# Optimization experiments

Measured on AMD Instinct MI355X. Metric: run time of the kernel, lower is better.

The kernel has to match this reference:

```python
import jax, jax.numpy as jnp
import numpy as np

B, N, C, R = 4, 4096, 64, 16
EPS = 1e-12


def setup_inputs() -> dict:
    key = jax.random.key(0)
    k_x, k_w, k_u = jax.random.split(key, 3)
    x = jax.random.normal(k_x, (B, N, C), dtype=jnp.float32)
    W = jax.random.uniform(k_w, (B, N, N), dtype=jnp.float32)
    # lazily-initialized learnable low-rank factor U ~ 0.01 * randn(N, r)
    U = 0.01 * jax.random.normal(k_u, (N, R), dtype=jnp.float32)
    w_scale = jnp.asarray(1.0, dtype=jnp.float32)
    return {"x": x, "W": W, "U": U, "w_scale": w_scale}


def reference(x, W, U, w_scale):
    # symmetrize adjacency: W <- (W + W^T)/2
    Ws = 0.5 * (W + jnp.swapaxes(W, -1, -2))            # [B,N,N]
    # low-rank symmetric gate A = sigmoid(U U^T), shared over batch
    A = jax.nn.sigmoid(U @ U.T)                          # [N,N]
    K = Ws * A[None, :, :]                               # [B,N,N]
    # degree normalization K <- D^{-1/2} K D^{-1/2}
    # (diag_embed + two bmms in the original == row/col broadcast scaling)
    deg = jnp.maximum(K.sum(axis=-1), EPS)               # [B,N]
    d = jax.lax.rsqrt(deg)                               # [B,N]
    K = K * d[:, :, None] * d[:, None, :]                # [B,N,N]
    # coupling: w_scale * K @ x
    return w_scale * jnp.einsum('bnm,bmc->bnc', K, x)    # [B,N,C]
```

## Files before the change

kernel.cpp:

```cpp
#include <hip/hip_runtime.h>
#include <hip/hip_bf16.h>

#define B_ 4
#define N_ 4096
#define C_ 64
#define R_ 16
#define EPS_ 1e-12f

typedef __attribute__((ext_vector_type(8))) short bf16x8;
typedef __attribute__((ext_vector_type(4))) float f32x4;

static __device__ __forceinline__ unsigned short f2bf(float f) {
    unsigned int u = __float_as_uint(f);
    unsigned int r = (u + 0x7fffu + ((u >> 16) & 1u)) >> 16;
    return (unsigned short)r;
}
static __device__ __forceinline__ float bf2f(unsigned short us) {
    return __uint_as_float(((unsigned int)us) << 16);
}

static __device__ __forceinline__ size_t k0f_off(int b, int rt, int k32, int fq, int fr) {
    return ((((size_t)(b * 256 + rt)) * 128 + k32) * 4 + fq) * 128 + fr * 8;
}

__global__ __launch_bounds__(256) void k_pass1(
    const float* __restrict__ W, const float* __restrict__ U,
    unsigned short* __restrict__ K0, float* __restrict__ deg)
{
    const int tj = blockIdx.x, ti = blockIdx.y;
    if (ti > tj) return;
    const int I = ti * 64, J = tj * 64;
    const bool diag = (ti == tj);
    const int t = threadIdx.x;
    const int ii = t >> 2, g = t & 3, jjg = g * 16;

    __shared__ float UJ[64][17];
    __shared__ float Wc[64][65];
    __shared__ __align__(16) unsigned short K0s[64][72];

    {
        const float4 v = *(const float4*)(U + (size_t)(J + (t >> 2)) * R_ + (t & 3) * 4);
        UJ[t >> 2][(t & 3) * 4 + 0] = v.x;
        UJ[t >> 2][(t & 3) * 4 + 1] = v.y;
        UJ[t >> 2][(t & 3) * 4 + 2] = v.z;
        UJ[t >> 2][(t & 3) * 4 + 3] = v.w;
    }

    float4 wcv[4], wrv[4], wcvN[4], wrvN[4];
    #pragma unroll
    for (int k = 0; k < 4; k++) {
        const int idx = t + 256 * k, row = idx >> 4, c4 = idx & 15;
        wcv[k] = *(const float4*)(W + ((size_t)(0 * N_ + J + row)) * N_ + I + c4 * 4);
    }
    #pragma unroll
    for (int h = 0; h < 4; h++)
        wrv[h] = *(const float4*)(W + ((size_t)(0 * N_ + I + ii)) * N_ + J + jjg + 4 * h);

    float ui[16];
    {
        const float* up = U + (size_t)(I + ii) * R_;
        #pragma unroll
        for (int h = 0; h < 4; h++) {
            float4 v = *(const float4*)(up + 4 * h);
            ui[4*h] = v.x; ui[4*h+1] = v.y; ui[4*h+2] = v.z; ui[4*h+3] = v.w;
        }
    }
    __syncthreads();

    float a[16];
    #pragma unroll
    for (int q = 0; q < 16; q++) {
        float s = 0.f;
        #pragma unroll
        for (int k = 0; k < 16; k++) s += ui[k] * UJ[jjg + q][k];
        a[q] = 1.0f / (1.0f + __expf(-s));
    }

    #pragma unroll
    for (int k = 0; k < 4; k++) {
        const int idx = t + 256 * k, row = idx >> 4, c4 = idx & 15;
        Wc[row][c4*4+0] = wcv[k].x; Wc[row][c4*4+1] = wcv[k].y;
        Wc[row][c4*4+2] = wcv[k].z; Wc[row][c4*4+3] = wcv[k].w;
    }
    __syncthreads();

    for (int b = 0; b < B_; b++) {
        if (b < B_ - 1) {
            #pragma unroll
            for (int k = 0; k < 4; k++) {
                const int idx = t + 256 * k, row = idx >> 4, c4 = idx & 15;
                wcvN[k] = *(const float4*)(W + ((size_t)((b+1) * N_ + J + row)) * N_ + I + c4 * 4);
            }
            #pragma unroll
            for (int h = 0; h < 4; h++)
                wrvN[h] = *(const float4*)(W + ((size_t)((b+1) * N_ + I + ii)) * N_ + J + jjg + 4 * h);
        }

        const float* wrf = (const float*)wrv;
        float sumI = 0.f;
        unsigned int pk[8];
        #pragma unroll
        for (int q = 0; q < 16; q++) {
            float k0 = 0.5f * (wrf[q] + Wc[jjg + q][ii]) * a[q];
            sumI += k0;
            unsigned short us = f2bf(k0);
            if (q & 1) pk[q >> 1] |= ((unsigned int)us) << 16;
            else       pk[q >> 1] = us;
        }
        *(int4*)(&K0s[ii][jjg])     = make_int4(pk[0], pk[1], pk[2], pk[3]);
        *(int4*)(&K0s[ii][jjg + 8]) = make_int4(pk[4], pk[5], pk[6], pk[7]);
        {
            const int rt  = (I + ii) >> 4, fr = ii & 15;
            const int k32 = (J >> 5) + (g >> 1), fqa = (g & 1) * 2;
            unsigned short* dst = K0 + k0f_off(b, rt, k32, fqa, fr);
            *(int4*)(dst)       = make_int4(pk[0], pk[1], pk[2], pk[3]);
            *(int4*)(dst + 128) = make_int4(pk[4], pk[5], pk[6], pk[7]);
        }
        {
            float s = sumI + __shfl_xor(sumI, 1, 64);
            s += __shfl_xor(s, 2, 64);
            if (g == 0) atomicAdd(deg + b * N_ + I + ii, s);
        }
        __syncthreads();

        if (!diag) {
            const int c2 = t & 31, r8 = t >> 5;
            unsigned int v[8];
            float cs0 = 0.f, cs1 = 0.f;
            #pragma unroll
            for (int k = 0; k < 8; k++) {
                v[k] = *(const unsigned int*)(&K0s[r8 * 8 + k][c2 * 2]);
                cs0 += bf2f((unsigned short)(v[k] & 0xffffu));
                cs1 += bf2f((unsigned short)(v[k] >> 16));
            }
            unsigned int plo[4], phi[4];
            #pragma unroll
            for (int m = 0; m < 4; m++) {
                plo[m] = (v[2*m] & 0xffffu) | (v[2*m+1] << 16);
                phi[m] = (v[2*m] >> 16) | (v[2*m+1] & 0xffff0000u);
            }
            const int rtp  = (J >> 4) + (c2 >> 3), fr0 = (2 * c2) & 15;
            const int k32p = (I >> 5) + (r8 >> 2), fqp = r8 & 3;
            unsigned short* dst0 = K0 + k0f_off(b, rtp, k32p, fqp, fr0);
            *(int4*)(dst0)     = make_int4(plo[0], plo[1], plo[2], plo[3]);
            *(int4*)(dst0 + 8) = make_int4(phi[0], phi[1], phi[2], phi[3]);
            cs0 += __shfl_xor(cs0, 32, 64);
            cs1 += __shfl_xor(cs1, 32, 64);
            if ((t & 32) == 0) {
                atomicAdd(deg + b * N_ + J + 2 * c2,     cs0);
                atomicAdd(deg + b * N_ + J + 2 * c2 + 1, cs1);
            }
        }
        if (b < B_ - 1) {
            #pragma unroll
            for (int k = 0; k < 4; k++) {
                const int idx = t + 256 * k, row = idx >> 4, c4 = idx & 15;
                Wc[row][c4*4+0] = wcvN[k].x; Wc[row][c4*4+1] = wcvN[k].y;
                Wc[row][c4*4+2] = wcvN[k].z; Wc[row][c4*4+3] = wcvN[k].w;
            }
            #pragma unroll
            for (int h = 0; h < 4; h++) wrv[h] = wrvN[h];
            __syncthreads();
        }
    }
}

__global__ __launch_bounds__(256) void k_xdT(
    const float* __restrict__ x, const float* __restrict__ deg,
    unsigned short* __restrict__ xdT)
{
    const int jt = blockIdx.x, b = blockIdx.y;
    const int J = jt * 64, t = threadIdx.x;
    __shared__ float xt[64][69];
    #pragma unroll
    for (int k = 0; k < 4; k++) {
        int idx = t + 256 * k;
        int row = idx >> 4, f4 = idx & 15;
        float d = rsqrtf(fmaxf(deg[b * N_ + J + row], EPS_));
        float4 v = *(const float4*)(x + ((size_t)(b * N_ + J + row)) * C_ + f4 * 4);
        xt[row][f4*4+0] = v.x * d; xt[row][f4*4+1] = v.y * d;
        xt[row][f4*4+2] = v.z * d; xt[row][f4*4+3] = v.w * d;
    }
    __syncthreads();
    #pragma unroll
    for (int p = 0; p < 2; p++) {
        const int linear = p * 256 + t;
        const int k32h = linear >> 8, rem = linear & 255;
        const int cg = rem >> 6, l = rem & 63, fq = l >> 4, fr = l & 15;
        const int c = cg * 16 + fr;
        const int jb = k32h * 32 + fq * 8;
        unsigned int pk[4];
        #pragma unroll
        for (int m = 0; m < 4; m++) {
            pk[m] = (unsigned int)f2bf(xt[jb + 2*m][c]) |
                    ((unsigned int)f2bf(xt[jb + 2*m + 1][c]) << 16);
        }
        unsigned short* dst = xdT +
            (((size_t)(b * 128 + (J >> 5) + k32h)) * 4 + cg) * 512 + l * 8;
        *(int4*)dst = make_int4(pk[0], pk[1], pk[2], pk[3]);
    }
}

__global__ __launch_bounds__(64, 4) void k_gemm(
    const unsigned short* __restrict__ K0, const unsigned short* __restrict__ xdT,
    const float* __restrict__ deg, const float* __restrict__ wsc_p,
    float* __restrict__ out)
{
    const int blk = blockIdx.x, b = blockIdx.y;
    const int rt = blk >> 2, kq = blk & 3;
    const int l = threadIdx.x;

    const unsigned short* Ap = K0  + (size_t)(b * 256 + rt) * 65536
                                   + (size_t)(kq * 32) * 512 + l * 8;
    const unsigned short* Bp = xdT + (size_t)b * 262144
                                   + (size_t)(kq * 32) * 2048 + l * 8;

    f32x4 acc0 = {0.f,0.f,0.f,0.f}, acc1 = {0.f,0.f,0.f,0.f};
    f32x4 acc2 = {0.f,0.f,0.f,0.f}, acc3 = {0.f,0.f,0.f,0.f};

    #pragma unroll 4
    for (int k = 0; k < 32; k++) {
        bf16x8 av = *(const bf16x8*)(Ap + (size_t)k * 512);
        bf16x8 b0 = *(const bf16x8*)(Bp + (size_t)k * 2048);
        bf16x8 b1 = *(const bf16x8*)(Bp + (size_t)k * 2048 + 512);
        bf16x8 b2 = *(const bf16x8*)(Bp + (size_t)k * 2048 + 1024);
        bf16x8 b3 = *(const bf16x8*)(Bp + (size_t)k * 2048 + 1536);
        acc0 = __builtin_amdgcn_mfma_f32_16x16x32_bf16(av, b0, acc0, 0, 0, 0);
        acc1 = __builtin_amdgcn_mfma_f32_16x16x32_bf16(av, b1, acc1, 0, 0, 0);
        acc2 = __builtin_amdgcn_mfma_f32_16x16x32_bf16(av, b2, acc2, 0, 0, 0);
        acc3 = __builtin_amdgcn_mfma_f32_16x16x32_bf16(av, b3, acc3, 0, 0, 0);
    }

    const int fr = l & 15, fq = l >> 4;
    const float wsc = wsc_p[0];
    #pragma unroll
    for (int r = 0; r < 4; r++) {
        const int row = rt * 16 + fq * 4 + r;
        const float sc = wsc * rsqrtf(fmaxf(deg[b * N_ + row], EPS_));
        float* op = out + ((size_t)(b * N_ + row)) * C_;
        atomicAdd(op + fr,      sc * acc0[r]);
        atomicAdd(op + 16 + fr, sc * acc1[r]);
        atomicAdd(op + 32 + fr, sc * acc2[r]);
        atomicAdd(op + 48 + fr, sc * acc3[r]);
    }
}

extern "C" void kernel_launch(void* const* d_in, const int* in_sizes, int n_in,
                              void* d_out, int out_size, void* d_ws, size_t ws_size,
                              hipStream_t stream)
{
    const float* x   = (const float*)d_in[0];
    const float* W   = (const float*)d_in[1];
    const float* U   = (const float*)d_in[2];
    const float* wsc = (const float*)d_in[3];
    float* out = (float*)d_out;

    unsigned short* K0  = (unsigned short*)d_ws;
    float*          deg = (float*)((char*)d_ws + (size_t)B_ * N_ * N_ * 2);
    unsigned short* xdT = (unsigned short*)((char*)deg + (size_t)B_ * N_ * 4);

    hipMemsetAsync(deg, 0, (size_t)B_ * N_ * sizeof(float), stream);
    hipMemsetAsync(out, 0, (size_t)B_ * N_ * C_ * sizeof(float), stream);
    hipLaunchKernelGGL(k_pass1, dim3(64, 64), dim3(256), 0, stream, W, U, K0, deg);
    hipLaunchKernelGGL(k_xdT,  dim3(64, 4),   dim3(256), 0, stream, x, deg, xdT);
    hipLaunchKernelGGL(k_gemm, dim3(1024, 4), dim3(64),  0, stream, K0, xdT, deg, wsc, out);
}
```

Measured before the change: 455.9 us.

## Restructure GEMM to LDS double-buffered full-K tiles without split-K atomics

The GEMM kernel now gives each 256-thread block two 16-row tiles over the full K range, in place of 64-thread blocks that split K four ways. A and B tiles are staged through double-buffered LDS with global_load_lds, which lets x-tile data be shared across waves. Each wave computes 16 rows by 32 columns. Because the whole K range is reduced inside one block, results are written directly instead of through atomicAdd, and the memset of the output is dropped. The costs are fewer blocks in flight (512 versus 4096) and two barriers per K step.

```diff
diff --git a/kernel.cpp b/kernel.cpp
--- a/kernel.cpp
+++ b/kernel.cpp
@@ -201,47 +201,103 @@
     }
 }
 
-__global__ __launch_bounds__(64, 4) void k_gemm(
+static __device__ __forceinline__ void gll16(const unsigned short* g, const unsigned short* l) {
+    __builtin_amdgcn_global_load_lds(
+        (const __attribute__((address_space(1))) unsigned int*)g,
+        (__attribute__((address_space(3))) unsigned int*)l,
+        16, 0, 0);
+}
+
+__global__ __launch_bounds__(256, 2) void k_gemm(
     const unsigned short* __restrict__ K0, const unsigned short* __restrict__ xdT,
     const float* __restrict__ deg, const float* __restrict__ wsc_p,
     float* __restrict__ out)
 {
-    const int blk = blockIdx.x, b = blockIdx.y;
-    const int rt = blk >> 2, kq = blk & 3;
-    const int l = threadIdx.x;
-
-    const unsigned short* Ap = K0  + (size_t)(b * 256 + rt) * 65536
-                                   + (size_t)(kq * 32) * 512 + l * 8;
-    const unsigned short* Bp = xdT + (size_t)b * 262144
-                                   + (size_t)(kq * 32) * 2048 + l * 8;
+    const int mg = blockIdx.x, b = blockIdx.y;
+    const int t = threadIdx.x, w = t >> 6, lane = t & 63;
+    const int rt0 = mg * 2;
+    const int rtl = w & 1, cgp = (w >> 1) * 2;
+    const int fq = lane >> 4, fr = lane & 15;
+    const int rt = rt0 + rtl;
+
+    __shared__ __align__(16) unsigned short As[2 * 8 * 512];
+    __shared__ __align__(16) unsigned short Bs[2 * 16 * 512];
+
+    const float wsc = wsc_p[0];
+    float dsc[4];
+    #pragma unroll
+    for (int r = 0; r < 4; r++)
+        dsc[r] = wsc * rsqrtf(fmaxf(deg[b * N_ + rt * 16 + fq * 4 + r], EPS_));
+
+    const unsigned short* gp[6];
+    const unsigned short* lp[6];
+    int ginc[6], linc[6];
+    #pragma unroll
+    for (int j = 0; j < 6; j++) {
+        const int id = w * 6 + j;
+        if (id < 8) {
+            const int art = id >> 2, c = id & 3;
+            gp[j] = K0 + (((size_t)(b * 256 + rt0 + art)) * 128 + c) * 512 + lane * 8;
+            lp[j] = As + id * 512;
+            ginc[j] = 4 * 512;
+            linc[j] = 8 * 512;
+        } else {
+            const int bi = id - 8, kc = bi >> 2, cg = bi & 3;
+            gp[j] = xdT + (((size_t)(b * 128 + kc)) * 4 + cg) * 512 + lane * 8;
+            lp[j] = Bs + bi * 512;
+            ginc[j] = 4 * 2048;
+            linc[j] = 16 * 512;
+        }
+    }
+
+    asm volatile("s_waitcnt vmcnt(0)" ::: "memory");
+    __builtin_amdgcn_sched_barrier(0);
+
+    #pragma unroll
+    for (int j = 0; j < 6; j++) {
+        gll16(gp[j], lp[j]);
+        gp[j] += ginc[j];
+    }
 
     f32x4 acc0 = {0.f,0.f,0.f,0.f}, acc1 = {0.f,0.f,0.f,0.f};
-    f32x4 acc2 = {0.f,0.f,0.f,0.f}, acc3 = {0.f,0.f,0.f,0.f};
-
-    #pragma unroll 4
-    for (int k = 0; k < 32; k++) {
-        bf16x8 av = *(const bf16x8*)(Ap + (size_t)k * 512);
-        bf16x8 b0 = *(const bf16x8*)(Bp + (size_t)k * 2048);
-        bf16x8 b1 = *(const bf16x8*)(Bp + (size_t)k * 2048 + 512);
-        bf16x8 b2 = *(const bf16x8*)(Bp + (size_t)k * 2048 + 1024);
-        bf16x8 b3 = *(const bf16x8*)(Bp + (size_t)k * 2048 + 1536);
-        acc0 = __builtin_amdgcn_mfma_f32_16x16x32_bf16(av, b0, acc0, 0, 0, 0);
-        acc1 = __builtin_amdgcn_mfma_f32_16x16x32_bf16(av, b1, acc1, 0, 0, 0);
-        acc2 = __builtin_amdgcn_mfma_f32_16x16x32_bf16(av, b2, acc2, 0, 0, 0);
-        acc3 = __builtin_amdgcn_mfma_f32_16x16x32_bf16(av, b3, acc3, 0, 0, 0);
-    }
-
-    const int fr = l & 15, fq = l >> 4;
-    const float wsc = wsc_p[0];
+    const int lo = lane * 8;
+    int cur = 0;
+
+    for (int t4 = 0; t4 < 32; t4++) {
+        if (t4 < 31) {
+            #pragma unroll
+            for (int j = 0; j < 6; j++) {
+                gll16(gp[j], lp[j] + (cur ? 0 : linc[j]));
+                gp[j] += ginc[j];
+            }
+        }
+        __builtin_amdgcn_sched_barrier(0);
+        if (t4 < 31) asm volatile("s_waitcnt vmcnt(6)" ::: "memory");
+        else         asm volatile("s_waitcnt vmcnt(0)" ::: "memory");
+        __builtin_amdgcn_s_barrier();
+        __builtin_amdgcn_sched_barrier(0);
+
+        const unsigned short* Ab = As + (cur ? 8 * 512 : 0) + rtl * 4 * 512 + lo;
+        const unsigned short* Bb = Bs + (cur ? 16 * 512 : 0) + cgp * 512 + lo;
+        #pragma unroll
+        for (int c = 0; c < 4; c++) {
+            bf16x8 av = *(const bf16x8*)(Ab + c * 512);
+            bf16x8 b0 = *(const bf16x8*)(Bb + c * 2048);
+            bf16x8 b1 = *(const bf16x8*)(Bb + c * 2048 + 512);
+            acc0 = __builtin_amdgcn_mfma_f32_16x16x32_bf16(av, b0, acc0, 0, 0, 0);
+            acc1 = __builtin_amdgcn_mfma_f32_16x16x32_bf16(av, b1, acc1, 0, 0, 0);
+        }
+        __builtin_amdgcn_sched_barrier(0);
+        __builtin_amdgcn_s_barrier();
+        cur ^= 1;
+    }
+
     #pragma unroll
     for (int r = 0; r < 4; r++) {
         const int row = rt * 16 + fq * 4 + r;
-        const float sc = wsc * rsqrtf(fmaxf(deg[b * N_ + row], EPS_));
         float* op = out + ((size_t)(b * N_ + row)) * C_;
-        atomicAdd(op + fr,      sc * acc0[r]);
-        atomicAdd(op + 16 + fr, sc * acc1[r]);
-        atomicAdd(op + 32 + fr, sc * acc2[r]);
-        atomicAdd(op + 48 + fr, sc * acc3[r]);
+        op[cgp * 16 + fr]      = dsc[r] * acc0[r];
+        op[cgp * 16 + 16 + fr] = dsc[r] * acc1[r];
     }
 }
 
@@ -260,8 +316,7 @@
     unsigned short* xdT = (unsigned short*)((char*)deg + (size_t)B_ * N_ * 4);
 
     hipMemsetAsync(deg, 0, (size_t)B_ * N_ * sizeof(float), stream);
-    hipMemsetAsync(out, 0, (size_t)B_ * N_ * C_ * sizeof(float), stream);
     hipLaunchKernelGGL(k_pass1, dim3(64, 64), dim3(256), 0, stream, W, U, K0, deg);
     hipLaunchKernelGGL(k_xdT,  dim3(64, 4),   dim3(256), 0, stream, x, deg, xdT);
-    hipLaunchKernelGGL(k_gemm, dim3(1024, 4), dim3(64),  0, stream, K0, xdT, deg, wsc, out);
-}
+    hipLaunchKernelGGL(k_gemm, dim3(128, 4),  dim3(256), 0, stream, K0, xdT, deg, wsc, out);
+}
```

After: 444.8 us. 1.02x faster.
